# Kernel tuning notes

Measured on AMD Instinct MI355X. Metric: run time of the kernel, lower is better.

## Reference

```python
import jax, jax.numpy as jnp
import numpy as np

N, E, F_IN, HID, H, NCLS, L = 100000, 1600000, 128, 128, 4, 40, 2
C = HID // H  # per-head channels = 32
LN_EPS = 1e-5
SOFTMAX_EPS = 1e-16  # PyG softmax denominator epsilon


def setup_inputs() -> dict:
    key = jax.random.key(0)
    ks = jax.random.split(key, 8)
    s = 1.0 / np.sqrt(F_IN).astype(np.float32)
    return {
        "x": jax.random.normal(ks[0], (N, F_IN), jnp.float32),
        "edge_index": jax.random.randint(ks[1], (2, E), 0, N, jnp.int32),
        "Wq": jax.random.normal(ks[2], (L, F_IN, HID), jnp.float32) * s,
        "bq": jnp.zeros((L, HID), jnp.float32),
        "Wk": jax.random.normal(ks[3], (L, F_IN, HID), jnp.float32) * s,
        "bk": jnp.zeros((L, HID), jnp.float32),
        "Wv": jax.random.normal(ks[4], (L, F_IN, HID), jnp.float32) * s,
        "bv": jnp.zeros((L, HID), jnp.float32),
        "Ws": jax.random.normal(ks[5], (L, F_IN, HID), jnp.float32) * s,
        "bs": jnp.zeros((L, HID), jnp.float32),
        "gamma": jnp.ones((L, HID), jnp.float32),
        "beta": jnp.zeros((L, HID), jnp.float32),
        "Wout": jax.random.normal(ks[6], (HID, NCLS), jnp.float32) * (1.0 / np.sqrt(HID).astype(np.float32)),
        "bout": jnp.zeros((NCLS,), jnp.float32),
    }


def _transformer_conv(x, src, dst, Wq, bq, Wk, bk, Wv, bv, Ws, bs):
    # PyG TransformerConv, concat=False, root_weight=True, beta=False
    n = x.shape[0]
    q = (x @ Wq + bq).reshape(n, H, C)
    k = (x @ Wk + bk).reshape(n, H, C)
    v = (x @ Wv + bv).reshape(n, H, C)
    # per-edge attention logits: [E, H]
    alpha = jnp.einsum('ehc,ehc->eh', q[dst], k[src]) / np.sqrt(C).astype(np.float32)
    # segment softmax over incoming edges of each destination node
    amax = jax.ops.segment_max(alpha, dst, num_segments=n)        # [N, H]
    ex = jnp.exp(alpha - amax[dst])                               # [E, H]
    denom = jax.ops.segment_sum(ex, dst, num_segments=n)         # [N, H]
    w = ex / (denom[dst] + SOFTMAX_EPS)                           # [E, H]
    msg = v[src] * w[:, :, None]                                  # [E, H, C]
    out = jax.ops.segment_sum(msg, dst, num_segments=n)          # [N, H, C]
    out = out.mean(axis=1)                                        # concat=False -> head average, [N, C*?]. Here C*H==HID only via mean over H of C dims -> [N, C]
    # NOTE: concat=False averages heads -> [N, C]; skip proj maps in->C? In PyG, out_channels=hidden here,
    # so lin_* are Linear(in, heads*hidden)... but TransformerConv(in, hidden) means out_channels=hidden/?
    return out


def _conv(x, src, dst, Wq, bq, Wk, bk, Wv, bv, Ws, bs):
    # Faithful version with out_channels = HID per head? No: TransformerConv(in, hidden, heads, concat=False)
    # in PyG uses out_channels=hidden and lin_* : in -> heads*out_channels. To keep HID total width we model
    # per-head dim C = HID // H (standard multi-head factorization with same total width HID).
    n = x.shape[0]
    q = (x @ Wq + bq).reshape(n, H, C)
    k = (x @ Wk + bk).reshape(n, H, C)
    v = (x @ Wv + bv).reshape(n, H, C)
    alpha = jnp.einsum('ehc,ehc->eh', q[dst], k[src]) / np.sqrt(C).astype(np.float32)
    amax = jax.ops.segment_max(alpha, dst, num_segments=n)
    ex = jnp.exp(alpha - amax[dst])
    denom = jax.ops.segment_sum(ex, dst, num_segments=n)
    w = ex / (denom[dst] + SOFTMAX_EPS)
    msg = (v[src] * w[:, :, None]).reshape(-1, H * C)             # [E, HID]
    agg = jax.ops.segment_sum(msg, dst, num_segments=n)          # [N, HID]
    # concat=False -> mean over heads, then broadcast back is not what PyG does; PyG yields [N, out_channels].
    out = agg.reshape(n, H, C).mean(axis=1)                       # [N, C]
    out = jnp.tile(out, (1, H))                                   # widen back to HID? No — instead use skip of width HID.
    return out


def _conv_layer(x, src, dst, Wq, bq, Wk, bk, Wv, bv, Ws, bs):
    """TransformerConv(in, HID, heads=H, concat=False): lin_{q,k,v}: in -> H*HID is too wide for a
    memory target, so we use the equivalent standard factorization HID = H*C (per-head C), giving
    attention output [N, H, C]; concat=False head-mean is applied per head group and the result is
    projected residually via lin_skip (in -> HID)."""
    n = x.shape[0]
    q = (x @ Wq + bq).reshape(n, H, C)
    k = (x @ Wk + bk).reshape(n, H, C)
    v = (x @ Wv + bv).reshape(n, H, C)
    alpha = jnp.einsum('ehc,ehc->eh', q[dst], k[src]) / np.sqrt(C).astype(np.float32)
    amax = jax.ops.segment_max(alpha, dst, num_segments=n)        # [N, H]
    ex = jnp.exp(alpha - amax[dst])                               # [E, H]
    denom = jax.ops.segment_sum(ex, dst, num_segments=n)
    w = ex / (denom[dst] + SOFTMAX_EPS)
    msg = (v[src] * w[:, :, None]).reshape(-1, HID)               # [E, HID] (head-concat)
    agg = jax.ops.segment_sum(msg, dst, num_segments=n)          # [N, HID]
    return agg + x @ Ws + bs                                      # root/skip connection


def _layernorm(h, g, b):
    mu = h.mean(-1, keepdims=True)
    var = ((h - mu) ** 2).mean(-1, keepdims=True)
    return (h - mu) * jax.lax.rsqrt(var + LN_EPS) * g + b


def reference(x, edge_index, Wq, bq, Wk, bk, Wv, bv, Ws, bs, gamma, beta, Wout, bout):
    src, dst = edge_index[0], edge_index[1]
    h = x
    for l in range(L):  # fixed small layer count
        h = _conv_layer(h, src, dst, Wq[l], bq[l], Wk[l], bk[l], Wv[l], bv[l], Ws[l], bs[l])
        h = jax.nn.relu(_layernorm(h, gamma[l], beta[l]))
        # dropout is identity in eval mode
    return h @ Wout + bout  # [N, NCLS]
```

## Files before the change

### kernel.cpp

```cpp
#include <hip/hip_runtime.h>
#include <math.h>

#define N_NODES 100000
#define N_EDGES 1600000
#define NCLS_ 40
#define NSCAN_BLOCKS ((N_NODES + 1023) / 1024)
#define SRCS_PAD (N_EDGES + 3 * N_NODES + 64)

#define QSCALE (0.17677669529663687f * 1.4426950408889634f)

#if __has_builtin(__builtin_amdgcn_exp2f)
#define EXP2(x) __builtin_amdgcn_exp2f(x)
#else
#define EXP2(x) exp2f(x)
#endif

typedef short bf16x8 __attribute__((ext_vector_type(8)));
typedef float f32x4 __attribute__((ext_vector_type(4)));

__device__ __forceinline__ unsigned short f2b(float f) {
    union { float f; unsigned u; } v; v.f = f;
    unsigned r = v.u + 0x7fffu + ((v.u >> 16) & 1u);
    return (unsigned short)(r >> 16);
}
__device__ __forceinline__ unsigned cvtpk(float x, float y) {
    unsigned r;
    asm("v_cvt_pk_bf16_f32 %0, %1, %2" : "=v"(r) : "v"(x), "v"(y));
    return r;
}
__device__ __forceinline__ float2 up2(unsigned u) {
    union { unsigned u; float f; } a, b;
    a.u = u << 16; b.u = u & 0xffff0000u;
    return make_float2(a.f, b.f);
}
__device__ __forceinline__ float b2f(unsigned short s) {
    union { unsigned u; float f; } v; v.u = ((unsigned)s) << 16;
    return v.f;
}


__global__ __launch_bounds__(256) void wconv_zero_kernel(
    const float* __restrict__ Wq, const float* __restrict__ Wk,
    const float* __restrict__ Wv, const float* __restrict__ Ws,
    unsigned short* __restrict__ Wbf, int* __restrict__ deg) {
    int b = blockIdx.x;
    if (b >= 512) {
        int i = (b - 512) * 256 + threadIdx.x;
        if (i < N_NODES) deg[i] = 0;
        return;
    }
    int tid = b * 256 + threadIdx.x;
    int j     = tid & 7;
    int lane  = (tid >> 3) & 63;
    int ks    = (tid >> 9) & 3;
    int c     = (tid >> 11) & 3;
    int ghalf = (tid >> 13) & 1;
    int mat   = (tid >> 14) & 3;
    int l     = tid >> 16;
    int ln = lane & 15, quad = lane >> 4;
    int col = ghalf * 64 + ((ln >> 2) << 4) + (c << 2) + (ln & 3);
    int krow = (ks << 5) + (quad << 3) + j;
    const float* W = (mat == 0) ? Wq : (mat == 1) ? Wk : (mat == 2) ? Wv : Ws;
    float w = W[l * 16384 + krow * 128 + col];
    if (mat == 0) w *= QSCALE;
    Wbf[tid] = f2b(w);
}

__global__ __launch_bounds__(256) void hist_kernel(
    const int* __restrict__ dst, int* __restrict__ deg) {
    int stride = gridDim.x * 256;
    for (int i = blockIdx.x * 256 + threadIdx.x; i < N_EDGES; i += stride)
        atomicAdd(&deg[dst[i]], 1);
}

__global__ __launch_bounds__(1024) void scan_block_kernel(
    const int* __restrict__ deg, int* __restrict__ rowptr, int* __restrict__ sums) {
    __shared__ int tmp[1024];
    int t = threadIdx.x;
    int i = blockIdx.x * 1024 + t;
    int v = (i < N_NODES) ? ((deg[i] + 3) & ~3) : 0;
    tmp[t] = v;
    __syncthreads();
    for (int d = 1; d < 1024; d <<= 1) {
        int add = (t >= d) ? tmp[t - d] : 0;
        __syncthreads();
        tmp[t] += add;
        __syncthreads();
    }
    if (i < N_NODES) rowptr[i] = tmp[t] - v;
    if (t == 1023) sums[blockIdx.x] = tmp[1023];
}

__global__ __launch_bounds__(256) void scan_add_kernel(
    int* __restrict__ rowptr, const int* __restrict__ sums,
    const int* __restrict__ deg,
    int* __restrict__ cursor, int* __restrict__ srcs) {
    __shared__ int base_s;
    int t = threadIdx.x;
    int limit = blockIdx.x >> 2;
    if (t < 64) {
        int v = (t < limit) ? sums[t] : 0;
        int v2 = (t + 64 < limit) ? sums[t + 64] : 0;
        v += v2;
        for (int m = 1; m < 64; m <<= 1) v += __shfl_xor(v, m);
        if (t == 0) base_s = v;
    }
    __syncthreads();
    int base = base_s;
    int i = blockIdx.x * 256 + t;
    if (i < N_NODES) {
        int val = rowptr[i] + base;
        rowptr[i] = val;
        cursor[i] = val;
        int d = deg[i];
        int pad = ((d + 3) & ~3);
        for (int j = d; j < pad; ++j) srcs[val + j] = 0;
        if (i == N_NODES - 1) {
            int end = val + pad;
            for (int j = 0; j < 16; ++j) srcs[end + j] = 0;
        }
    }
}

__global__ __launch_bounds__(256) void scatter_kernel(
    const int* __restrict__ src, const int* __restrict__ dst,
    int* __restrict__ cursor, int* __restrict__ srcs) {
    int stride = gridDim.x * 256;
    for (int i = blockIdx.x * 256 + threadIdx.x; i < N_EDGES; i += stride) {
        int pos = atomicAdd(&cursor[dst[i]], 1);
        srcs[pos] = src[i] << 10;
    }
}

__global__ __launch_bounds__(512, 4) void gemm_qkvs_kernel(
    const void* __restrict__ Ap, int a_is_bf16,
    const unsigned short* __restrict__ Wbf,
    const float* __restrict__ b0, const float* __restrict__ b1,
    const float* __restrict__ b2, const float* __restrict__ b3,
    unsigned short* __restrict__ out) {
    __shared__ unsigned short WL[2][8192];
    int t = threadIdx.x;
    int row0 = blockIdx.x * 128;
    int wr = t >> 6, lane = t & 63;
    int ln = lane & 15, quad = lane >> 4;
    int node = row0 + wr * 16 + ln;
    int nodeC = (node < N_NODES) ? node : (N_NODES - 1);

    bf16x8 aF[4];
    if (a_is_bf16) {
        const unsigned short* ar = (const unsigned short*)Ap + (size_t)nodeC * 128;
        #pragma unroll
        for (int ks = 0; ks < 4; ++ks)
            aF[ks] = *(const bf16x8*)&ar[ks * 32 + quad * 8];
    } else {
        const float* ar = (const float*)Ap + (size_t)nodeC * 128;
        #pragma unroll
        for (int ks = 0; ks < 4; ++ks) {
            float4 f0 = *(const float4*)&ar[ks * 32 + quad * 8];
            float4 f1 = *(const float4*)&ar[ks * 32 + quad * 8 + 4];
            union { unsigned u[4]; bf16x8 v; } cv;
            cv.u[0] = cvtpk(f0.x, f0.y);
            cv.u[1] = cvtpk(f0.z, f0.w);
            cv.u[2] = cvtpk(f1.x, f1.y);
            cv.u[3] = cvtpk(f1.z, f1.w);
            aF[ks] = cv.v;
        }
    }

    {
        const uint4* Wg4 = (const uint4*)Wbf;
        uint4 a = Wg4[t * 2], b = Wg4[t * 2 + 1];
        uint4* d4 = (uint4*)WL[0] + t * 2;
        d4[0] = a; d4[1] = b;
    }
    __syncthreads();

    bool ok = node < N_NODES;
    #pragma unroll
    for (int g = 0; g < 8; ++g) {
        int mat = g >> 1;
        int cur = g & 1;
        const float* bias = (mat == 0) ? b0 : (mat == 1) ? b1 : (mat == 2) ? b2 : b3;
        int cb = (g & 1) * 64;

        uint4 pfa, pfb;
        if (g < 7) {
            const uint4* Wg4 = (const uint4*)(Wbf + (size_t)(g + 1) * 8192);
            pfa = Wg4[t * 2]; pfb = Wg4[t * 2 + 1];
        }

        f32x4 acc[4];
        #pragma unroll
        for (int c = 0; c < 4; ++c) acc[c] = (f32x4){0.f, 0.f, 0.f, 0.f};
        #pragma unroll
        for (int ks = 0; ks < 4; ++ks) {
            #pragma unroll
            for (int c = 0; c < 4; ++c) {
                bf16x8 w = *(bf16x8*)&WL[cur][((c * 4 + ks) * 64 + lane) * 8];
                acc[c] = __builtin_amdgcn_mfma_f32_16x16x32_bf16(w, aF[ks], acc[c], 0, 0, 0);
            }
        }

        if (ok) {
            float s = (mat == 0) ? QSCALE : 1.0f;
            float v[16];
            #pragma unroll
            for (int c = 0; c < 4; ++c) {
                float4 bb = *(const float4*)&bias[cb + quad * 16 + c * 4];
                v[c * 4 + 0] = acc[c][0] + bb.x * s;
                v[c * 4 + 1] = acc[c][1] + bb.y * s;
                v[c * 4 + 2] = acc[c][2] + bb.z * s;
                v[c * 4 + 3] = acc[c][3] + bb.w * s;
            }
            unsigned pk[8];
            #pragma unroll
            for (int m = 0; m < 8; ++m) pk[m] = cvtpk(v[2 * m], v[2 * m + 1]);
            unsigned short* orow = out + (size_t)node * 512;
            if (mat == 0 || mat == 3) {
                int base = (mat == 0 ? 0 : 384) + cb + quad * 16;
                uint4 w0 = make_uint4(pk[0], pk[1], pk[2], pk[3]);
                uint4 w1 = make_uint4(pk[4], pk[5], pk[6], pk[7]);
                *(uint4*)&orow[base] = w0;
                *(uint4*)&orow[base + 8] = w1;
            } else {
                int boff = (mat == 2) ? 4 : 0;
                #pragma unroll
                for (int c = 0; c < 4; ++c) {
                    int pos = 128 + 8 * ((cb >> 2) + quad * 4 + c) + boff;
                    uint2 wd; wd.x = pk[2 * c]; wd.y = pk[2 * c + 1];
                    *(uint2*)&orow[pos] = wd;
                }
            }
        }

        if (g < 7) {
            uint4* d4 = (uint4*)WL[cur ^ 1] + t * 2;
            d4[0] = pfa; d4[1] = pfb;
        }
        __syncthreads();
    }
}

#define EDGE(KV, ECOND) {                                            \
        float2 k01 = up2(KV.x), k23 = up2(KV.y);                     \
        float p = q01.x*k01.x + q01.y*k01.y + q23.x*k23.x + q23.y*k23.y; \
        p += __shfl_xor(p, 1);                                       \
        p += __shfl_xor(p, 2);                                       \
        p += __shfl_xor(p, 4);                                       \
        float e = (ECOND);                                           \
        float2 v01 = up2(KV.z), v23 = up2(KV.w);                     \
        a0 = fmaf(e, v01.x, a0); a1 = fmaf(e, v01.y, a1);            \
        a2 = fmaf(e, v23.x, a2); a3 = fmaf(e, v23.y, a3);            \
        dsum += e; }

__global__ __launch_bounds__(256) void edge_fused_kernel(
    const unsigned short* __restrict__ qkvs,
    const int* __restrict__ srcs, const int* __restrict__ rowptr,
    const int* __restrict__ deg,
    const float* __restrict__ gamma, const float* __restrict__ beta,
    unsigned short* __restrict__ hout) {
    int n = (blockIdx.x * 256 + threadIdx.x) >> 6;
    int lane = threadIdx.x & 63;
    if (n >= N_NODES) return;
    int half = lane >> 5, hl = lane & 31;
    const unsigned short* qrow = qkvs + (size_t)n * 512;
    uint2 qu = *(const uint2*)&qrow[4 * hl];
    float2 q01 = up2(qu.x), q23 = up2(qu.y);
    uint2 su = *(const uint2*)&qrow[384 + 4 * hl];
    float2 sk01 = up2(su.x), sk23 = up2(su.y);
    int e0 = rowptr[n];
    int rem = deg[n];
    const char* kbase = (const char*)qkvs + 256 + 16 * hl;
    const int* sb = srcs + e0 + 4 * half;
    float a0 = 0.f, a1 = 0.f, a2 = 0.f, a3 = 0.f, dsum = 0.f;

    int4 oc;
    if (rem >= 8) oc = *(const int4*)sb;
    while (rem >= 8) {
        int4 on;
        if (rem >= 16) on = *(const int4*)(sb + 8);
        uint4 kv0 = *(const uint4*)(kbase + (unsigned)oc.x);
        uint4 kv1 = *(const uint4*)(kbase + (unsigned)oc.y);
        uint4 kv2 = *(const uint4*)(kbase + (unsigned)oc.z);
        uint4 kv3 = *(const uint4*)(kbase + (unsigned)oc.w);
        EDGE(kv0, EXP2(p));
        EDGE(kv1, EXP2(p));
        EDGE(kv2, EXP2(p));
        EDGE(kv3, EXP2(p));
        oc = on; sb += 8; rem -= 8;
    }
    if (rem > 0) {
        int4 ot = *(const int4*)sb;
        int tb = 4 * half;
        uint4 kv0 = *(const uint4*)(kbase + (unsigned)ot.x);
        uint4 kv1 = *(const uint4*)(kbase + (unsigned)ot.y);
        uint4 kv2 = *(const uint4*)(kbase + (unsigned)ot.z);
        uint4 kv3 = *(const uint4*)(kbase + (unsigned)ot.w);
        EDGE(kv0, (tb + 0 < rem) ? EXP2(p) : 0.f);
        EDGE(kv1, (tb + 1 < rem) ? EXP2(p) : 0.f);
        EDGE(kv2, (tb + 2 < rem) ? EXP2(p) : 0.f);
        EDGE(kv3, (tb + 3 < rem) ? EXP2(p) : 0.f);
    }

    a0 += __shfl_xor(a0, 32); a1 += __shfl_xor(a1, 32);
    a2 += __shfl_xor(a2, 32); a3 += __shfl_xor(a3, 32);
    dsum += __shfl_xor(dsum, 32);
    float dinv = 1.0f / (dsum + 1e-16f);
    float o0 = a0 * dinv + sk01.x, o1 = a1 * dinv + sk01.y;
    float o2 = a2 * dinv + sk23.x, o3 = a3 * dinv + sk23.y;
    float sum = o0 + o1 + o2 + o3;
    for (int m = 1; m < 64; m <<= 1) sum += __shfl_xor(sum, m);
    float mu = sum * (1.0f / 256.0f);
    float d0 = o0 - mu, d1 = o1 - mu, d2 = o2 - mu, d3 = o3 - mu;
    float sq = d0 * d0 + d1 * d1 + d2 * d2 + d3 * d3;
    for (int m = 1; m < 64; m <<= 1) sq += __shfl_xor(sq, m);
    float rs = rsqrtf(sq * (1.0f / 256.0f) + 1e-5f);
    if (half == 0) {
        float4 g4 = *(const float4*)&gamma[4 * hl];
        float4 b4 = *(const float4*)&beta[4 * hl];
        float r0 = fmaxf(d0 * rs * g4.x + b4.x, 0.f);
        float r1 = fmaxf(d1 * rs * g4.y + b4.y, 0.f);
        float r2 = fmaxf(d2 * rs * g4.z + b4.z, 0.f);
        float r3 = fmaxf(d3 * rs * g4.w + b4.w, 0.f);
        uint2 w;
        w.x = cvtpk(r0, r1);
        w.y = cvtpk(r2, r3);
        *(uint2*)&hout[(size_t)n * 128 + 4 * hl] = w;
    }
}

__global__ __launch_bounds__(256) void out_gemm_kernel(
    const unsigned short* __restrict__ h, const float* __restrict__ Wout,
    const float* __restrict__ bout, float* __restrict__ out) {
    int wv = __builtin_amdgcn_readfirstlane((int)(threadIdx.x >> 6));
    int l = threadIdx.x & 63;
    int n = blockIdx.x * 64 + l;
    int jb = wv * 10;
    int nc = (n < N_NODES) ? n : (N_NODES - 1);
    const unsigned short* hrow = h + (size_t)nc * 128;
    uint4 hp[16];
    #pragma unroll
    for (int i = 0; i < 16; ++i) hp[i] = *(const uint4*)&hrow[i * 8];
    float acc[10];
    #pragma unroll
    for (int j = 0; j < 10; ++j) acc[j] = bout[jb + j];
    #pragma unroll
    for (int i = 0; i < 16; ++i) {
        float2 c01 = up2(hp[i].x), c23 = up2(hp[i].y);
        float2 c45 = up2(hp[i].z), c67 = up2(hp[i].w);
        float hc0 = c01.x, hc1 = c01.y, hc2 = c23.x, hc3 = c23.y;
        float hc4 = c45.x, hc5 = c45.y, hc6 = c67.x, hc7 = c67.y;
        #pragma unroll
        for (int j = 0; j < 10; ++j) {
            const float* wk = Wout + (i * 8) * NCLS_ + jb + j;
            acc[j] = fmaf(hc0, wk[0 * NCLS_], acc[j]);
            acc[j] = fmaf(hc1, wk[1 * NCLS_], acc[j]);
            acc[j] = fmaf(hc2, wk[2 * NCLS_], acc[j]);
            acc[j] = fmaf(hc3, wk[3 * NCLS_], acc[j]);
            acc[j] = fmaf(hc4, wk[4 * NCLS_], acc[j]);
            acc[j] = fmaf(hc5, wk[5 * NCLS_], acc[j]);
            acc[j] = fmaf(hc6, wk[6 * NCLS_], acc[j]);
            acc[j] = fmaf(hc7, wk[7 * NCLS_], acc[j]);
        }
    }
    if (n < N_NODES) {
        #pragma unroll
        for (int j = 0; j < 10; ++j) out[(size_t)n * NCLS_ + jb + j] = acc[j];
    }
}

extern "C" void kernel_launch(void* const* d_in, const int* in_sizes, int n_in,
                              void* d_out, int out_size, void* d_ws, size_t ws_size,
                              hipStream_t stream) {
    const float* x    = (const float*)d_in[0];
    const int*   ei   = (const int*)d_in[1];
    const int*   src  = ei;
    const int*   dst  = ei + N_EDGES;
    const float* Wq   = (const float*)d_in[2];
    const float* bq   = (const float*)d_in[3];
    const float* Wk   = (const float*)d_in[4];
    const float* bk   = (const float*)d_in[5];
    const float* Wv   = (const float*)d_in[6];
    const float* bv   = (const float*)d_in[7];
    const float* Wsk  = (const float*)d_in[8];
    const float* bsk  = (const float*)d_in[9];
    const float* gmm  = (const float*)d_in[10];
    const float* bta  = (const float*)d_in[11];
    const float* Wout = (const float*)d_in[12];
    const float* bout = (const float*)d_in[13];
    float* outp = (float*)d_out;

    char* p = (char*)d_ws;
    auto carve = [&](size_t bytes) {
        char* r = p;
        p += (bytes + 255) & ~(size_t)255;
        return r;
    };
    unsigned short* qkvs = (unsigned short*)carve((size_t)N_NODES * 512 * 2);
    unsigned short* h    = (unsigned short*)carve((size_t)N_NODES * 128 * 2);
    unsigned short* Wbf  = (unsigned short*)carve((size_t)131072 * 2);
    int* deg     = (int*)carve((size_t)N_NODES * 4);
    int* rowptr  = (int*)carve((size_t)(N_NODES + 1) * 4);
    int* cursor  = (int*)carve((size_t)N_NODES * 4);
    int* srcs    = (int*)carve((size_t)SRCS_PAD * 4);
    int* sums    = (int*)carve((size_t)NSCAN_BLOCKS * 4);

    wconv_zero_kernel<<<512 + (N_NODES + 255) / 256, 256, 0, stream>>>(
        Wq, Wk, Wv, Wsk, Wbf, deg);
    hist_kernel<<<2048, 256, 0, stream>>>(dst, deg);
    scan_block_kernel<<<NSCAN_BLOCKS, 1024, 0, stream>>>(deg, rowptr, sums);
    scan_add_kernel<<<(N_NODES + 255) / 256, 256, 0, stream>>>(rowptr, sums, deg, cursor, srcs);
    scatter_kernel<<<2048, 256, 0, stream>>>(src, dst, cursor, srcs);

    for (int l = 0; l < 2; ++l) {
        const void* hin = l ? (const void*)h : (const void*)x;
        gemm_qkvs_kernel<<<(N_NODES + 127) / 128, 512, 0, stream>>>(
            hin, l, Wbf + (size_t)l * 65536,
            bq + l * 128, bk + l * 128, bv + l * 128, bsk + l * 128, qkvs);
        edge_fused_kernel<<<(N_NODES + 3) / 4, 256, 0, stream>>>(
            qkvs, srcs, rowptr, deg, gmm + l * 128, bta + l * 128, h);
    }
    out_gemm_kernel<<<(N_NODES + 63) / 64, 256, 0, stream>>>(h, Wout, bout, outp);
}
```

Measured before the change: 692.0 us.

## Partition CSR build atomics by destination range and software-pipeline edge gathers

The histogram and scatter kernels now split blocks into 8 groups, each handling only destinations in its own 12500-node range, so atomics from a group land in a smaller, more cache-local region. The cost is that every group reads the whole dst array. The attention aggregation loop is software-pipelined: the gathered K/V rows for the next 8 edges are loaded before the current ones are processed, with the index prefetch moved one step further ahead, to hide gather latency. This uses more registers and could lower occupancy.

Measured after the change: 663.6 us. 4.1% less time.

```diff
diff --git a/kernel.cpp b/kernel.cpp
--- a/kernel.cpp
+++ b/kernel.cpp
@@ -5,6 +5,7 @@
 #define N_EDGES 1600000
 #define NCLS_ 40
 #define NSCAN_BLOCKS ((N_NODES + 1023) / 1024)
+#define DRANGE 12500
 #define SRCS_PAD (N_EDGES + 3 * N_NODES + 64)
 
 #define QSCALE (0.17677669529663687f * 1.4426950408889634f)
@@ -68,9 +69,14 @@
 
 __global__ __launch_bounds__(256) void hist_kernel(
     const int* __restrict__ dst, int* __restrict__ deg) {
-    int stride = gridDim.x * 256;
-    for (int i = blockIdx.x * 256 + threadIdx.x; i < N_EDGES; i += stride)
-        atomicAdd(&deg[dst[i]], 1);
+    int group = blockIdx.x & 7;
+    int gblk  = blockIdx.x >> 3;
+    int nblk  = gridDim.x >> 3;
+    int lo = group * DRANGE, hi = lo + DRANGE;
+    for (int i = gblk * 256 + threadIdx.x; i < N_EDGES; i += nblk * 256) {
+        int d = dst[i];
+        if (d >= lo && d < hi) atomicAdd(&deg[d], 1);
+    }
 }
 
 __global__ __launch_bounds__(1024) void scan_block_kernel(
@@ -125,10 +131,16 @@
 __global__ __launch_bounds__(256) void scatter_kernel(
     const int* __restrict__ src, const int* __restrict__ dst,
     int* __restrict__ cursor, int* __restrict__ srcs) {
-    int stride = gridDim.x * 256;
-    for (int i = blockIdx.x * 256 + threadIdx.x; i < N_EDGES; i += stride) {
-        int pos = atomicAdd(&cursor[dst[i]], 1);
-        srcs[pos] = src[i] << 10;
+    int group = blockIdx.x & 7;
+    int gblk  = blockIdx.x >> 3;
+    int nblk  = gridDim.x >> 3;
+    int lo = group * DRANGE, hi = lo + DRANGE;
+    for (int i = gblk * 256 + threadIdx.x; i < N_EDGES; i += nblk * 256) {
+        int d = dst[i];
+        if (d >= lo && d < hi) {
+            int pos = atomicAdd(&cursor[d], 1);
+            srcs[pos] = src[i] << 10;
+        }
     }
 }
 
@@ -274,20 +286,36 @@
     const int* sb = srcs + e0 + 4 * half;
     float a0 = 0.f, a1 = 0.f, a2 = 0.f, a3 = 0.f, dsum = 0.f;
 
-    int4 oc;
-    if (rem >= 8) oc = *(const int4*)sb;
-    while (rem >= 8) {
-        int4 on;
+    uint4 c0, c1, c2, c3;
+    int4 on;
+    if (rem >= 8) {
+        int4 oc = *(const int4*)sb;
+        c0 = *(const uint4*)(kbase + (unsigned)oc.x);
+        c1 = *(const uint4*)(kbase + (unsigned)oc.y);
+        c2 = *(const uint4*)(kbase + (unsigned)oc.z);
+        c3 = *(const uint4*)(kbase + (unsigned)oc.w);
         if (rem >= 16) on = *(const int4*)(sb + 8);
-        uint4 kv0 = *(const uint4*)(kbase + (unsigned)oc.x);
-        uint4 kv1 = *(const uint4*)(kbase + (unsigned)oc.y);
-        uint4 kv2 = *(const uint4*)(kbase + (unsigned)oc.z);
-        uint4 kv3 = *(const uint4*)(kbase + (unsigned)oc.w);
-        EDGE(kv0, EXP2(p));
-        EDGE(kv1, EXP2(p));
-        EDGE(kv2, EXP2(p));
-        EDGE(kv3, EXP2(p));
-        oc = on; sb += 8; rem -= 8;
+    }
+    while (rem >= 16) {
+        uint4 n0 = *(const uint4*)(kbase + (unsigned)on.x);
+        uint4 n1 = *(const uint4*)(kbase + (unsigned)on.y);
+        uint4 n2 = *(const uint4*)(kbase + (unsigned)on.z);
+        uint4 n3 = *(const uint4*)(kbase + (unsigned)on.w);
+        int4 of = *(const int4*)(sb + 16);
+        EDGE(c0, EXP2(p));
+        EDGE(c1, EXP2(p));
+        EDGE(c2, EXP2(p));
+        EDGE(c3, EXP2(p));
+        c0 = n0; c1 = n1; c2 = n2; c3 = n3;
+        on = of;
+        sb += 8; rem -= 8;
+    }
+    if (rem >= 8) {
+        EDGE(c0, EXP2(p));
+        EDGE(c1, EXP2(p));
+        EDGE(c2, EXP2(p));
+        EDGE(c3, EXP2(p));
+        sb += 8; rem -= 8;
     }
     if (rem > 0) {
         int4 ot = *(const int4*)sb;
```
